# Kernel optimization log

Measured on AMD Instinct MI355X. Metric: run time of the kernel, lower is better.

## Reference

```python
import jax, jax.numpy as jnp
import numpy as np
import math

N, E, G = 10000, 100000, 500
HID, H = 128, 4
C = HID                      # out_channels per head (PyG TransformerConv)
NFREQ, NSPACE = 10, 3
EDIM = 2 * NFREQ * NSPACE    # 60 = dis_emb.dim
LAT, DIS = 6, 3
IN_DIM = HID + LAT + DIS     # 137
EPS = 1e-5


def _lin_init(k, fan_in, shape):
    b = 1.0 / math.sqrt(fan_in)
    return jax.random.uniform(k, shape, jnp.float32, -b, b)


def setup_inputs() -> dict:
    key = jax.random.key(0)
    ks = jax.random.split(key, 12)
    return dict(
        node_features=jax.random.normal(ks[0], (N, HID), jnp.float32),
        frac_coords=jax.random.uniform(ks[1], (N, DIS), jnp.float32),
        lattice_feats=jax.random.normal(ks[2], (G, LAT), jnp.float32),
        edge_index=jax.random.randint(ks[3], (2, E), 0, N),
        node2graph=jnp.sort(jax.random.randint(ks[4], (N,), 0, G)),
        frac_diff=jax.random.normal(ks[5], (E, DIS), jnp.float32) * 0.1,
        ln_gamma=jnp.ones((HID,), jnp.float32),
        ln_beta=jnp.zeros((HID,), jnp.float32),
        Wq=_lin_init(ks[6], IN_DIM, (IN_DIM, H * C)), bq=jnp.zeros((H * C,), jnp.float32),
        Wk=_lin_init(ks[7], IN_DIM, (IN_DIM, H * C)), bk=jnp.zeros((H * C,), jnp.float32),
        Wv=_lin_init(ks[8], IN_DIM, (IN_DIM, H * C)), bv=jnp.zeros((H * C,), jnp.float32),
        We=_lin_init(ks[9], EDIM, (EDIM, H * C)),
        Wskip=_lin_init(ks[10], IN_DIM, (IN_DIM, C)), bskip=jnp.zeros((C,), jnp.float32),
    )


def _sinusoids(frac_diff):
    # SinusoidsEmbedding: emb = x[...,None]*2*pi*arange(F); cat(sin, cos); detached
    freqs = 2.0 * jnp.pi * jnp.arange(NFREQ, dtype=jnp.float32)    # [F]
    emb = frac_diff[:, :, None] * freqs[None, None, :]             # [E,3,F]
    emb = emb.reshape(-1, NSPACE * NFREQ)                          # [E,30]
    return jnp.concatenate([jnp.sin(emb), jnp.cos(emb)], axis=-1)  # [E,60]


def _segment_softmax(scores, idx, num_segments):
    # softmax over variable-size neighborhoods grouped by target node idx
    m = jax.ops.segment_max(scores, idx, num_segments=num_segments)
    ex = jnp.exp(scores - m[idx])
    s = jax.ops.segment_sum(ex, idx, num_segments=num_segments)
    return ex / (s[idx] + 1e-16)


def reference(node_features, frac_coords, lattice_feats, edge_index, node2graph,
              frac_diff, ln_gamma, ln_beta, Wq, bq, Wk, bk, Wv, bv, We, Wskip, bskip):
    edge_emb = jax.lax.stop_gradient(_sinusoids(frac_diff))  # .detach() in original
    node_input = node_features
    # LayerNorm (biased variance, torch default)
    mu = node_features.mean(-1, keepdims=True)
    var = node_features.var(-1, keepdims=True)
    h = (node_features - mu) * jax.lax.rsqrt(var + EPS) * ln_gamma + ln_beta
    # gather per-graph lattice features to nodes, concat
    lat = lattice_feats.reshape(-1, LAT)[node2graph]                # [N,6]
    x = jnp.concatenate([h, lat, frac_coords], axis=1)              # [N,137]

    q = (x @ Wq + bq).reshape(N, H, C)
    k = (x @ Wk + bk).reshape(N, H, C)
    v = (x @ Wv + bv).reshape(N, H, C)
    e = (edge_emb @ We).reshape(E, H, C)                            # lin_edge (no bias)

    src, dst = edge_index[0], edge_index[1]  # message flows src -> dst (PyG default)
    k_e = k[src] + e                                                # [E,H,C]
    alpha = (q[dst] * k_e).sum(-1) / math.sqrt(C)                   # [E,H]
    alpha = _segment_softmax(alpha, dst, N)
    msg = (v[src] + e) * alpha[:, :, None]                          # [E,H,C]
    out = jax.ops.segment_sum(msg, dst, num_segments=N)             # [N,H,C]
    out = out.mean(axis=1)                                          # concat=False -> head mean
    out = out + (x @ Wskip + bskip)                                 # root skip connection
    return node_input + jax.nn.silu(out)
```

## Files before the change

kernel.cpp:

```cpp
#include <hip/hip_runtime.h>
#include <math.h>

#define N_NODES 10000
#define N_EDGES 100000
#define HIDDEN  128
#define NHEAD   4
#define CHAN    128
#define IN_DIM  137
#define KPAD    160
#define NCOLS   1904
#define NPAD    1920
#define LATD    6
#define DISD    3

typedef __attribute__((ext_vector_type(8))) short short8v;
typedef __attribute__((ext_vector_type(4))) float float4v;

__device__ inline unsigned short f2bf(float f) {
    unsigned u = __float_as_uint(f);
    unsigned r = 0x7fffu + ((u >> 16) & 1u);
    return (unsigned short)((u + r) >> 16);
}
__device__ inline float bf2f(unsigned short u) {
    return __uint_as_float(((unsigned)u) << 16);
}

__global__ __launch_bounds__(256) void hist_kernel(
    const int* __restrict__ eidx, int* __restrict__ hist)
{
    int e = blockIdx.x * 256 + threadIdx.x;
    if (e < N_EDGES) atomicAdd(&hist[eidx[N_EDGES + e]], 1);
}

__global__ __launch_bounds__(1024) void scan_kernel(
    const int* __restrict__ hist, int* __restrict__ offsets, int* __restrict__ cursor)
{
    __shared__ int part[1024];
    const int t = threadIdx.x;
    const int base = t * 10;
    int loc[10];
    int s = 0;
    #pragma unroll
    for (int i = 0; i < 10; ++i) {
        int v = (base + i < N_NODES) ? hist[base + i] : 0;
        loc[i] = s; s += v;
    }
    part[t] = s;
    __syncthreads();
    for (int off = 1; off < 1024; off <<= 1) {
        int v = (t >= off) ? part[t - off] : 0;
        __syncthreads();
        part[t] += v;
        __syncthreads();
    }
    int pre = (t > 0) ? part[t - 1] : 0;
    #pragma unroll
    for (int i = 0; i < 10; ++i)
        if (base + i < N_NODES) {
            offsets[base + i] = pre + loc[i];
            cursor[base + i]  = pre + loc[i];
        }
    if (t == 1023) offsets[N_NODES] = part[1023];
}

__global__ __launch_bounds__(256) void scatter_kernel(
    const int* __restrict__ eidx, const float* __restrict__ fdiff,
    int* __restrict__ cursor, int* __restrict__ sorted_src,
    float* __restrict__ sorted_fd)
{
    int e = blockIdx.x * 256 + threadIdx.x;
    if (e >= N_EDGES) return;
    int src = eidx[e];
    int dst = eidx[N_EDGES + e];
    int pos = atomicAdd(&cursor[dst], 1);
    sorted_src[pos] = src;
    sorted_fd[pos * 3 + 0] = fdiff[e * 3 + 0];
    sorted_fd[pos * 3 + 1] = fdiff[e * 3 + 1];
    sorted_fd[pos * 3 + 2] = fdiff[e * 3 + 2];
}

__global__ __launch_bounds__(256) void prep_kernel(
    const float* __restrict__ nf, const float* __restrict__ frac,
    const float* __restrict__ lat, const int* __restrict__ n2g,
    const float* __restrict__ gamma, const float* __restrict__ beta,
    unsigned short* __restrict__ xb, int* __restrict__ hist)
{
    int wave = threadIdx.x >> 6;
    int lane = threadIdx.x & 63;
    int n = blockIdx.x * 4 + wave;
    if (n >= N_NODES) return;

    float v0 = nf[n * HIDDEN + lane];
    float v1 = nf[n * HIDDEN + 64 + lane];
    float s  = v0 + v1;
    float sq = v0 * v0 + v1 * v1;
    #pragma unroll
    for (int m = 1; m < 64; m <<= 1) {
        s  += __shfl_xor(s, m);
        sq += __shfl_xor(sq, m);
    }
    float mean = s * (1.0f / 128.0f);
    float var  = sq * (1.0f / 128.0f) - mean * mean;
    float inv  = rsqrtf(var + 1e-5f);

    xb[n * KPAD + lane]      = f2bf((v0 - mean) * inv * gamma[lane]      + beta[lane]);
    xb[n * KPAD + 64 + lane] = f2bf((v1 - mean) * inv * gamma[64 + lane] + beta[64 + lane]);
    if (lane < LATD) xb[n * KPAD + HIDDEN + lane]        = f2bf(lat[n2g[n] * LATD + lane]);
    if (lane < DISD) xb[n * KPAD + HIDDEN + LATD + lane] = f2bf(frac[n * DISD + lane]);
    if (lane >= 41)  xb[n * KPAD + 96 + lane] = 0;
    if (lane == 0)   hist[n] = 0;
}

__global__ __launch_bounds__(256) void weights_kernel(
    const float* __restrict__ Wq, const float* __restrict__ bq,
    const float* __restrict__ Wk, const float* __restrict__ bk,
    const float* __restrict__ Wv, const float* __restrict__ bv,
    const float* __restrict__ Wsk, const float* __restrict__ bsk,
    const float* __restrict__ We,
    unsigned short* __restrict__ wallT, float* __restrict__ bias_all,
    unsigned short* __restrict__ webt)
{
    int idx = blockIdx.x * 256 + threadIdx.x;
    if (idx < NCOLS * KPAD) {
        int n = idx / KPAD, k = idx % KPAD;
        if (n < 1664) {
            float val = 0.0f;
            if (k < IN_DIM) {
                if (n < 512)        val = Wq[(size_t)k * 512 + n];
                else if (n < 1024)  val = Wk[(size_t)k * 512 + (n - 512)];
                else if (n < 1536)  val = Wv[(size_t)k * 512 + (n - 1024)];
                else                val = Wsk[(size_t)k * 128 + (n - 1536)];
            }
            wallT[idx] = f2bf(val);
            if (k == 0) {
                float b;
                if (n < 512)        b = bq[n];
                else if (n < 1024)  b = bk[n - 512];
                else if (n < 1536)  b = bv[n - 1024];
                else                b = bsk[n - 1536];
                bias_all[n] = b;
            }
        } else {
            int hj = n - 1664;
            int h = hj / 60, j = hj % 60;
            float s = 0.0f;
            if (k < IN_DIM) {
                #pragma unroll 4
                for (int c = 0; c < 128; ++c)
                    s += Wq[(size_t)k * 512 + h * 128 + c] * We[(size_t)j * 512 + h * 128 + c];
            }
            wallT[idx] = f2bf(s);
            if (k == KPAD - 1) {
                float b = 0.0f;
                #pragma unroll 4
                for (int c = 0; c < 128; ++c)
                    b += bq[h * 128 + c] * We[(size_t)j * 512 + h * 128 + c];
                bias_all[n] = b;
            }
        }
    } else {
        int g = idx - NCOLS * KPAD;
        int h = g >> 13, c = (g >> 6) & 127, j = g & 63;
        float v = (j < 60) ? We[(size_t)j * 512 + h * 128 + c] : 0.0f;
        webt[g] = f2bf(v);
    }
}

__global__ __launch_bounds__(256) void mfma_gemm_kernel(
    const unsigned short* __restrict__ xb, const unsigned short* __restrict__ wallT,
    const float* __restrict__ bias_all,
    float* __restrict__ qsq, unsigned short* __restrict__ kvq)
{
    __shared__ __align__(16) unsigned short Alds[64 * 168];
    const int row0 = blockIdx.y * 64;
    const int col0 = blockIdx.x * 128;
    const int tid  = threadIdx.x;

    for (int i = tid; i < 64 * 20; i += 256) {
        int r = i / 20, c8 = (i % 20) * 8;
        uint4 v = make_uint4(0u, 0u, 0u, 0u);
        if (row0 + r < N_NODES)
            v = *reinterpret_cast<const uint4*>(&xb[(size_t)(row0 + r) * KPAD + c8]);
        *reinterpret_cast<uint4*>(&Alds[r * 168 + c8]) = v;
    }
    __syncthreads();

    const int l   = tid & 63;
    const int wid = tid >> 6;
    const int wr  = (wid >> 1) * 32;
    const int wc  = (wid & 1) * 64;
    const int lr  = l & 15;
    const int lk  = (l >> 4) * 8;

    float4v acc[2][4];
    #pragma unroll
    for (int tr = 0; tr < 2; ++tr)
        #pragma unroll
        for (int tc = 0; tc < 4; ++tc)
            acc[tr][tc] = (float4v){0.0f, 0.0f, 0.0f, 0.0f};

    #pragma unroll
    for (int ks = 0; ks < 5; ++ks) {
        short8v a[2], b[4];
        #pragma unroll
        for (int t = 0; t < 2; ++t)
            a[t] = *reinterpret_cast<const short8v*>(&Alds[(wr + t * 16 + lr) * 168 + ks * 32 + lk]);
        #pragma unroll
        for (int t = 0; t < 4; ++t)
            b[t] = *reinterpret_cast<const short8v*>(
                &wallT[(size_t)(col0 + wc + t * 16 + lr) * KPAD + ks * 32 + lk]);
        #pragma unroll
        for (int tr = 0; tr < 2; ++tr)
            #pragma unroll
            for (int tc = 0; tc < 4; ++tc)
                acc[tr][tc] = __builtin_amdgcn_mfma_f32_16x16x32_bf16(a[tr], b[tc], acc[tr][tc], 0, 0, 0);
    }

    #pragma unroll
    for (int tr = 0; tr < 2; ++tr) {
        #pragma unroll
        for (int tc = 0; tc < 4; ++tc) {
            const int col  = col0 + wc + tc * 16 + lr;
            const float bias = bias_all[col];
            #pragma unroll
            for (int j = 0; j < 4; ++j) {
                const int row = row0 + wr + tr * 16 + (l >> 4) * 4 + j;
                if (row < N_NODES) {
                    float val = acc[tr][tc][j] + bias;
                    if (col < 1536)
                        kvq[(size_t)row * 1536 + col] = f2bf(val);
                    else if (col < NCOLS)
                        qsq[(size_t)row * 880 + (col - 1024)] = val;
                }
            }
        }
    }
}

__global__ __launch_bounds__(256) void gather_kernel(
    float* __restrict__ qsq, const unsigned short* __restrict__ kvq,
    const int* __restrict__ offsets, const int* __restrict__ sorted_src,
    const float* __restrict__ sorted_fd)
{
    const int n    = blockIdx.x;
    const int h    = threadIdx.x >> 6;
    const int l    = threadIdx.x & 63;
    const int hl   = l & 31;
    const int half = l >> 5;
    const float TWO_PI = 6.283185307179586f;
    const float scale  = 0.08838834764831845f;

    float* row = qsq + (size_t)n * 880;
    const ushort4 qv = *reinterpret_cast<const ushort4*>(
        &kvq[(size_t)n * 1536 + h * 128 + 4 * hl]);
    const float q4x = bf2f(qv.x), q4y = bf2f(qv.y);
    const float q4z = bf2f(qv.z), q4w = bf2f(qv.w);
    const float qe_a = row[640 + h * 60 + hl];
    const bool  v2ok = (hl < 28);
    const float qe_b = v2ok ? row[640 + h * 60 + hl + 32] : 0.0f;

    const int   jj1  = (hl < 30) ? hl : hl - 30;
    const int   sd1  = jj1 / 10;
    const float fc1  = TWO_PI * (float)(jj1 % 10);
    const bool  sin1 = (hl < 30);
    const int   jj2  = hl + 2;
    const int   sd2  = v2ok ? (jj2 / 10) : 0;
    const float fc2  = v2ok ? TWO_PI * (float)(jj2 % 10) : 0.0f;

    float ax = 0.f, ay = 0.f, az = 0.f, aw = 0.f;
    float agg1 = 0.f, agg2 = 0.f, sumw = 0.f;
    const int e0 = offsets[n], e1 = offsets[n + 1];

    for (int base = e0; base < e1; base += 4) {
        const int eA = base + half;
        const int eB = base + half + 2;
        const bool okA = (eA < e1), okB = (eB < e1);
        const int iA = okA ? eA : e0;
        const int iB = okB ? eB : e0;
        const int srcA = sorted_src[iA];
        const int srcB = sorted_src[iB];
        const float fdA1 = sorted_fd[iA * 3 + sd1];
        const float fdA2 = sorted_fd[iA * 3 + sd2];
        const float fdB1 = sorted_fd[iB * 3 + sd1];
        const float fdB2 = sorted_fd[iB * 3 + sd2];
        const unsigned short* pA = &kvq[(size_t)srcA * 1536 + 512 + h * 128 + 4 * hl];
        const unsigned short* pB = &kvq[(size_t)srcB * 1536 + 512 + h * 128 + 4 * hl];
        const ushort4 kA = *reinterpret_cast<const ushort4*>(pA);
        const ushort4 vA = *reinterpret_cast<const ushort4*>(pA + 512);
        const ushort4 kB = *reinterpret_cast<const ushort4*>(pB);
        const ushort4 vB = *reinterpret_cast<const ushort4*>(pB + 512);

        const float eA1 = sin1 ? __sinf(fdA1 * fc1) : __cosf(fdA1 * fc1);
        const float eA2 = __cosf(fdA2 * fc2);
        const float eB1 = sin1 ? __sinf(fdB1 * fc1) : __cosf(fdB1 * fc1);
        const float eB2 = __cosf(fdB2 * fc2);

        float pAs = q4x * bf2f(kA.x) + q4y * bf2f(kA.y)
                  + q4z * bf2f(kA.z) + q4w * bf2f(kA.w)
                  + eA1 * qe_a + eA2 * qe_b;
        float pBs = q4x * bf2f(kB.x) + q4y * bf2f(kB.y)
                  + q4z * bf2f(kB.z) + q4w * bf2f(kB.w)
                  + eB1 * qe_a + eB2 * qe_b;
        #pragma unroll
        for (int m = 1; m <= 16; m <<= 1) {
            pAs += __shfl_xor(pAs, m);
            pBs += __shfl_xor(pBs, m);
        }
        const float wA = okA ? __expf(pAs * scale) : 0.0f;
        const float wB = okB ? __expf(pBs * scale) : 0.0f;
        sumw += wA + wB;
        ax += wA * bf2f(vA.x) + wB * bf2f(vB.x);
        ay += wA * bf2f(vA.y) + wB * bf2f(vB.y);
        az += wA * bf2f(vA.z) + wB * bf2f(vB.z);
        aw += wA * bf2f(vA.w) + wB * bf2f(vB.w);
        agg1 += wA * eA1 + wB * eB1;
        if (v2ok) agg2 += wA * eA2 + wB * eB2;
    }

    sumw += __shfl_xor(sumw, 32);
    ax += __shfl_xor(ax, 32);  ay += __shfl_xor(ay, 32);
    az += __shfl_xor(az, 32);  aw += __shfl_xor(aw, 32);
    agg1 += __shfl_xor(agg1, 32);
    agg2 += __shfl_xor(agg2, 32);

    __syncthreads();

    if (half == 0) {
        float4 r;
        r.x = ax; r.y = ay; r.z = az; r.w = aw;
        *reinterpret_cast<float4*>(&row[h * 128 + 4 * hl]) = r;
        unsigned short* us = (unsigned short*)(row + 640);
        us[h * 64 + hl]      = f2bf(agg1);
        us[h * 64 + 32 + hl] = f2bf(agg2);
        if (hl == 0) row[768 + h] = sumw;
    }
}

__global__ __launch_bounds__(256) void corr_kernel(
    const unsigned short* __restrict__ webt, float* __restrict__ qsq)
{
    __shared__ __align__(16) unsigned short Alds[32 * 264];
    const int node0 = blockIdx.x * 32;
    const int tid = threadIdx.x;

    for (int i = tid; i < 32 * 32; i += 256) {
        int r = i >> 5, c8 = (i & 31) * 8;
        uint4 v = make_uint4(0u, 0u, 0u, 0u);
        if (node0 + r < N_NODES)
            v = *reinterpret_cast<const uint4*>(
                (const unsigned short*)(qsq + (size_t)(node0 + r) * 880 + 640) + c8);
        *reinterpret_cast<uint4*>(&Alds[r * 264 + c8]) = v;
    }
    __syncthreads();

    const int l  = tid & 63;
    const int h  = tid >> 6;
    const int lr = l & 15;
    const int lk = (l >> 4) * 8;

    float4v acc[2][8];
    #pragma unroll
    for (int m = 0; m < 2; ++m)
        #pragma unroll
        for (int nn = 0; nn < 8; ++nn)
            acc[m][nn] = (float4v){0.0f, 0.0f, 0.0f, 0.0f};

    #pragma unroll
    for (int ks = 0; ks < 2; ++ks) {
        short8v a[2], b[8];
        #pragma unroll
        for (int m = 0; m < 2; ++m)
            a[m] = *reinterpret_cast<const short8v*>(
                &Alds[(m * 16 + lr) * 264 + h * 64 + ks * 32 + lk]);
        #pragma unroll
        for (int nn = 0; nn < 8; ++nn)
            b[nn] = *reinterpret_cast<const short8v*>(
                &webt[(size_t)(h * 128 + nn * 16 + lr) * 64 + ks * 32 + lk]);
        #pragma unroll
        for (int m = 0; m < 2; ++m)
            #pragma unroll
            for (int nn = 0; nn < 8; ++nn)
                acc[m][nn] = __builtin_amdgcn_mfma_f32_16x16x32_bf16(a[m], b[nn], acc[m][nn], 0, 0, 0);
    }

    #pragma unroll
    for (int m = 0; m < 2; ++m) {
        #pragma unroll
        for (int nn = 0; nn < 8; ++nn) {
            const int col = h * 128 + nn * 16 + lr;
            #pragma unroll
            for (int j = 0; j < 4; ++j) {
                const int rowi = node0 + m * 16 + (l >> 4) * 4 + j;
                if (rowi < N_NODES) {
                    float* p = &qsq[(size_t)rowi * 880 + col];
                    *p += acc[m][nn][j];
                }
            }
        }
    }
}

__global__ __launch_bounds__(256) void finalize_kernel(
    const float* __restrict__ qsq, const float* __restrict__ nf,
    float* __restrict__ out)
{
    int idx = blockIdx.x * 256 + threadIdx.x;
    if (idx >= N_NODES * CHAN) return;
    int n = idx >> 7, c = idx & 127;
    const float* row = qsq + (size_t)n * 880;
    float z = 0.0f;
    #pragma unroll
    for (int h = 0; h < NHEAD; ++h)
        z += row[h * 128 + c] / (row[768 + h] + 1e-16f);
    z = 0.25f * z + row[512 + c];
    float si = z / (1.0f + __expf(-z));
    out[idx] = nf[idx] + si;
}

extern "C" void kernel_launch(void* const* d_in, const int* in_sizes, int n_in,
                              void* d_out, int out_size, void* d_ws, size_t ws_size,
                              hipStream_t stream)
{
    const float* nf    = (const float*)d_in[0];
    const float* frac  = (const float*)d_in[1];
    const float* lat   = (const float*)d_in[2];
    const int*   eidx  = (const int*)  d_in[3];
    const int*   n2g   = (const int*)  d_in[4];
    const float* fdiff = (const float*)d_in[5];
    const float* gamma = (const float*)d_in[6];
    const float* beta  = (const float*)d_in[7];
    const float* Wq    = (const float*)d_in[8];
    const float* bq    = (const float*)d_in[9];
    const float* Wk    = (const float*)d_in[10];
    const float* bk    = (const float*)d_in[11];
    const float* Wv    = (const float*)d_in[12];
    const float* bv    = (const float*)d_in[13];
    const float* We    = (const float*)d_in[14];
    const float* Wsk   = (const float*)d_in[15];
    const float* bsk   = (const float*)d_in[16];
    float* out = (float*)d_out;

    float* qsq       = (float*)d_ws;
    float* bias_all  = qsq + (size_t)N_NODES * 880;
    float* sorted_fd = bias_all + NPAD;
    unsigned short* xb    = (unsigned short*)(sorted_fd + (size_t)N_EDGES * 3);
    unsigned short* wallT = xb + (size_t)N_NODES * KPAD;
    unsigned short* webt  = wallT + (size_t)NPAD * KPAD;
    unsigned short* kvq   = webt + 4 * 128 * 64;
    int* hist       = (int*)(kvq + (size_t)N_NODES * 1536);
    int* offsets    = hist + N_NODES;
    int* cursor     = offsets + N_NODES + 1;
    int* sorted_src = cursor + N_NODES;

    prep_kernel<<<(N_NODES + 3) / 4, 256, 0, stream>>>(
        nf, frac, lat, n2g, gamma, beta, xb, hist);
    hist_kernel<<<(N_EDGES + 255) / 256, 256, 0, stream>>>(eidx, hist);
    scan_kernel<<<1, 1024, 0, stream>>>(hist, offsets, cursor);
    scatter_kernel<<<(N_EDGES + 255) / 256, 256, 0, stream>>>(
        eidx, fdiff, cursor, sorted_src, sorted_fd);

    weights_kernel<<<(NCOLS * KPAD + 4 * 128 * 64) / 256, 256, 0, stream>>>(
        Wq, bq, Wk, bk, Wv, bv, Wsk, bsk, We, wallT, bias_all, webt);

    dim3 ggrid(NPAD / 128, (N_NODES + 63) / 64);
    mfma_gemm_kernel<<<ggrid, 256, 0, stream>>>(xb, wallT, bias_all, qsq, kvq);

    gather_kernel<<<N_NODES, 256, 0, stream>>>(
        qsq, kvq, offsets, sorted_src, sorted_fd);

    corr_kernel<<<(N_NODES + 31) / 32, 256, 0, stream>>>(webt, qsq);

    finalize_kernel<<<(N_NODES * CHAN + 255) / 256, 256, 0, stream>>>(
        qsq, nf, out);
}
```

Baseline: 147.7 us.

## Fuse prep with weights packing and corr with finalize, split workspace buffers

Merges the layernorm prep and weight packing into one launch using block-index ranges, and fuses the edge-correction MFMA with the final head-mean, skip-add and SiLU via a shared-memory accumulator. The packed qsq row is split into separate buffers (skip/qe, av, agg, sumw), so gather no longer rewrites the row it reads and its block barrier is removed. This cuts two kernel launches and a full read-modify-write pass over the per-node rows. In exchange, corrfin serialises its four head waves through a phased loop with a barrier per phase.

```diff
diff --git a/kernel.cpp b/kernel.cpp
--- a/kernel.cpp
+++ b/kernel.cpp
@@ -13,6 +13,10 @@
 #define LATD    6
 #define DISD    3
 
+#define PREP_BLOCKS 2500
+#define WTOT   (NCOLS * KPAD + 4 * 128 * 64)
+#define WBLOCKS ((WTOT + 255) / 256)
+
 typedef __attribute__((ext_vector_type(8))) short short8v;
 typedef __attribute__((ext_vector_type(4))) float float4v;
 
@@ -23,6 +27,93 @@
 }
 __device__ inline float bf2f(unsigned short u) {
     return __uint_as_float(((unsigned)u) << 16);
+}
+
+__global__ __launch_bounds__(256) void prep_weights_kernel(
+    const float* __restrict__ nf, const float* __restrict__ frac,
+    const float* __restrict__ lat, const int* __restrict__ n2g,
+    const float* __restrict__ gamma, const float* __restrict__ beta,
+    const float* __restrict__ Wq, const float* __restrict__ bq,
+    const float* __restrict__ Wk, const float* __restrict__ bk,
+    const float* __restrict__ Wv, const float* __restrict__ bv,
+    const float* __restrict__ Wsk, const float* __restrict__ bsk,
+    const float* __restrict__ We,
+    unsigned short* __restrict__ xb, int* __restrict__ hist,
+    unsigned short* __restrict__ wallT, float* __restrict__ bias_all,
+    unsigned short* __restrict__ webt)
+{
+    if (blockIdx.x < PREP_BLOCKS) {
+        int wave = threadIdx.x >> 6;
+        int lane = threadIdx.x & 63;
+        int n = blockIdx.x * 4 + wave;
+        if (n >= N_NODES) return;
+
+        float v0 = nf[n * HIDDEN + lane];
+        float v1 = nf[n * HIDDEN + 64 + lane];
+        float s  = v0 + v1;
+        float sq = v0 * v0 + v1 * v1;
+        #pragma unroll
+        for (int m = 1; m < 64; m <<= 1) {
+            s  += __shfl_xor(s, m);
+            sq += __shfl_xor(sq, m);
+        }
+        float mean = s * (1.0f / 128.0f);
+        float var  = sq * (1.0f / 128.0f) - mean * mean;
+        float inv  = rsqrtf(var + 1e-5f);
+
+        xb[n * KPAD + lane]      = f2bf((v0 - mean) * inv * gamma[lane]      + beta[lane]);
+        xb[n * KPAD + 64 + lane] = f2bf((v1 - mean) * inv * gamma[64 + lane] + beta[64 + lane]);
+        if (lane < LATD) xb[n * KPAD + HIDDEN + lane]        = f2bf(lat[n2g[n] * LATD + lane]);
+        if (lane < DISD) xb[n * KPAD + HIDDEN + LATD + lane] = f2bf(frac[n * DISD + lane]);
+        if (lane >= 41)  xb[n * KPAD + 96 + lane] = 0;
+        if (lane == 0)   hist[n] = 0;
+    } else {
+        int idx = (blockIdx.x - PREP_BLOCKS) * 256 + threadIdx.x;
+        if (idx >= WTOT) return;
+        if (idx < NCOLS * KPAD) {
+            int n = idx / KPAD, k = idx % KPAD;
+            if (n < 1664) {
+                float val = 0.0f;
+                if (k < IN_DIM) {
+                    if (n < 512)        val = Wq[(size_t)k * 512 + n];
+                    else if (n < 1024)  val = Wk[(size_t)k * 512 + (n - 512)];
+                    else if (n < 1536)  val = Wv[(size_t)k * 512 + (n - 1024)];
+                    else                val = Wsk[(size_t)k * 128 + (n - 1536)];
+                }
+                wallT[idx] = f2bf(val);
+                if (k == 0) {
+                    float b;
+                    if (n < 512)        b = bq[n];
+                    else if (n < 1024)  b = bk[n - 512];
+                    else if (n < 1536)  b = bv[n - 1024];
+                    else                b = bsk[n - 1536];
+                    bias_all[n] = b;
+                }
+            } else {
+                int hj = n - 1664;
+                int h = hj / 60, j = hj % 60;
+                float s = 0.0f;
+                if (k < IN_DIM) {
+                    #pragma unroll 4
+                    for (int c = 0; c < 128; ++c)
+                        s += Wq[(size_t)k * 512 + h * 128 + c] * We[(size_t)j * 512 + h * 128 + c];
+                }
+                wallT[idx] = f2bf(s);
+                if (k == KPAD - 1) {
+                    float b = 0.0f;
+                    #pragma unroll 4
+                    for (int c = 0; c < 128; ++c)
+                        b += bq[h * 128 + c] * We[(size_t)j * 512 + h * 128 + c];
+                    bias_all[n] = b;
+                }
+            }
+        } else {
+            int g = idx - NCOLS * KPAD;
+            int h = g >> 13, c = (g >> 6) & 127, j = g & 63;
+            float v = (j < 60) ? We[(size_t)j * 512 + h * 128 + c] : 0.0f;
+            webt[g] = f2bf(v);
+        }
+    }
 }
 
 __global__ __launch_bounds__(256) void hist_kernel(
@@ -79,97 +170,10 @@
     sorted_fd[pos * 3 + 2] = fdiff[e * 3 + 2];
 }
 
-__global__ __launch_bounds__(256) void prep_kernel(
-    const float* __restrict__ nf, const float* __restrict__ frac,
-    const float* __restrict__ lat, const int* __restrict__ n2g,
-    const float* __restrict__ gamma, const float* __restrict__ beta,
-    unsigned short* __restrict__ xb, int* __restrict__ hist)
-{
-    int wave = threadIdx.x >> 6;
-    int lane = threadIdx.x & 63;
-    int n = blockIdx.x * 4 + wave;
-    if (n >= N_NODES) return;
-
-    float v0 = nf[n * HIDDEN + lane];
-    float v1 = nf[n * HIDDEN + 64 + lane];
-    float s  = v0 + v1;
-    float sq = v0 * v0 + v1 * v1;
-    #pragma unroll
-    for (int m = 1; m < 64; m <<= 1) {
-        s  += __shfl_xor(s, m);
-        sq += __shfl_xor(sq, m);
-    }
-    float mean = s * (1.0f / 128.0f);
-    float var  = sq * (1.0f / 128.0f) - mean * mean;
-    float inv  = rsqrtf(var + 1e-5f);
-
-    xb[n * KPAD + lane]      = f2bf((v0 - mean) * inv * gamma[lane]      + beta[lane]);
-    xb[n * KPAD + 64 + lane] = f2bf((v1 - mean) * inv * gamma[64 + lane] + beta[64 + lane]);
-    if (lane < LATD) xb[n * KPAD + HIDDEN + lane]        = f2bf(lat[n2g[n] * LATD + lane]);
-    if (lane < DISD) xb[n * KPAD + HIDDEN + LATD + lane] = f2bf(frac[n * DISD + lane]);
-    if (lane >= 41)  xb[n * KPAD + 96 + lane] = 0;
-    if (lane == 0)   hist[n] = 0;
-}
-
-__global__ __launch_bounds__(256) void weights_kernel(
-    const float* __restrict__ Wq, const float* __restrict__ bq,
-    const float* __restrict__ Wk, const float* __restrict__ bk,
-    const float* __restrict__ Wv, const float* __restrict__ bv,
-    const float* __restrict__ Wsk, const float* __restrict__ bsk,
-    const float* __restrict__ We,
-    unsigned short* __restrict__ wallT, float* __restrict__ bias_all,
-    unsigned short* __restrict__ webt)
-{
-    int idx = blockIdx.x * 256 + threadIdx.x;
-    if (idx < NCOLS * KPAD) {
-        int n = idx / KPAD, k = idx % KPAD;
-        if (n < 1664) {
-            float val = 0.0f;
-            if (k < IN_DIM) {
-                if (n < 512)        val = Wq[(size_t)k * 512 + n];
-                else if (n < 1024)  val = Wk[(size_t)k * 512 + (n - 512)];
-                else if (n < 1536)  val = Wv[(size_t)k * 512 + (n - 1024)];
-                else                val = Wsk[(size_t)k * 128 + (n - 1536)];
-            }
-            wallT[idx] = f2bf(val);
-            if (k == 0) {
-                float b;
-                if (n < 512)        b = bq[n];
-                else if (n < 1024)  b = bk[n - 512];
-                else if (n < 1536)  b = bv[n - 1024];
-                else                b = bsk[n - 1536];
-                bias_all[n] = b;
-            }
-        } else {
-            int hj = n - 1664;
-            int h = hj / 60, j = hj % 60;
-            float s = 0.0f;
-            if (k < IN_DIM) {
-                #pragma unroll 4
-                for (int c = 0; c < 128; ++c)
-                    s += Wq[(size_t)k * 512 + h * 128 + c] * We[(size_t)j * 512 + h * 128 + c];
-            }
-            wallT[idx] = f2bf(s);
-            if (k == KPAD - 1) {
-                float b = 0.0f;
-                #pragma unroll 4
-                for (int c = 0; c < 128; ++c)
-                    b += bq[h * 128 + c] * We[(size_t)j * 512 + h * 128 + c];
-                bias_all[n] = b;
-            }
-        }
-    } else {
-        int g = idx - NCOLS * KPAD;
-        int h = g >> 13, c = (g >> 6) & 127, j = g & 63;
-        float v = (j < 60) ? We[(size_t)j * 512 + h * 128 + c] : 0.0f;
-        webt[g] = f2bf(v);
-    }
-}
-
 __global__ __launch_bounds__(256) void mfma_gemm_kernel(
     const unsigned short* __restrict__ xb, const unsigned short* __restrict__ wallT,
     const float* __restrict__ bias_all,
-    float* __restrict__ qsq, unsigned short* __restrict__ kvq)
+    float* __restrict__ sq, unsigned short* __restrict__ kvq)
 {
     __shared__ __align__(16) unsigned short Alds[64 * 168];
     const int row0 = blockIdx.y * 64;
@@ -229,8 +233,10 @@
                     float val = acc[tr][tc][j] + bias;
                     if (col < 1536)
                         kvq[(size_t)row * 1536 + col] = f2bf(val);
+                    else if (col < 1664)
+                        sq[(size_t)row * 384 + (col - 1536)] = val;
                     else if (col < NCOLS)
-                        qsq[(size_t)row * 880 + (col - 1024)] = val;
+                        sq[(size_t)row * 384 + 128 + (col - 1664)] = val;
                 }
             }
         }
@@ -238,9 +244,11 @@
 }
 
 __global__ __launch_bounds__(256) void gather_kernel(
-    float* __restrict__ qsq, const unsigned short* __restrict__ kvq,
+    const float* __restrict__ sq, const unsigned short* __restrict__ kvq,
     const int* __restrict__ offsets, const int* __restrict__ sorted_src,
-    const float* __restrict__ sorted_fd)
+    const float* __restrict__ sorted_fd,
+    float* __restrict__ avbuf, unsigned short* __restrict__ aggbuf,
+    float* __restrict__ sumwbuf)
 {
     const int n    = blockIdx.x;
     const int h    = threadIdx.x >> 6;
@@ -250,14 +258,13 @@
     const float TWO_PI = 6.283185307179586f;
     const float scale  = 0.08838834764831845f;
 
-    float* row = qsq + (size_t)n * 880;
     const ushort4 qv = *reinterpret_cast<const ushort4*>(
         &kvq[(size_t)n * 1536 + h * 128 + 4 * hl]);
     const float q4x = bf2f(qv.x), q4y = bf2f(qv.y);
     const float q4z = bf2f(qv.z), q4w = bf2f(qv.w);
-    const float qe_a = row[640 + h * 60 + hl];
+    const float qe_a = sq[(size_t)n * 384 + 128 + h * 60 + hl];
     const bool  v2ok = (hl < 28);
-    const float qe_b = v2ok ? row[640 + h * 60 + hl + 32] : 0.0f;
+    const float qe_b = v2ok ? sq[(size_t)n * 384 + 128 + h * 60 + hl + 32] : 0.0f;
 
     const int   jj1  = (hl < 30) ? hl : hl - 30;
     const int   sd1  = jj1 / 10;
@@ -323,23 +330,24 @@
     agg1 += __shfl_xor(agg1, 32);
     agg2 += __shfl_xor(agg2, 32);
 
-    __syncthreads();
-
     if (half == 0) {
         float4 r;
         r.x = ax; r.y = ay; r.z = az; r.w = aw;
-        *reinterpret_cast<float4*>(&row[h * 128 + 4 * hl]) = r;
-        unsigned short* us = (unsigned short*)(row + 640);
-        us[h * 64 + hl]      = f2bf(agg1);
-        us[h * 64 + 32 + hl] = f2bf(agg2);
-        if (hl == 0) row[768 + h] = sumw;
-    }
-}
-
-__global__ __launch_bounds__(256) void corr_kernel(
-    const unsigned short* __restrict__ webt, float* __restrict__ qsq)
+        *reinterpret_cast<float4*>(&avbuf[(size_t)n * 512 + h * 128 + 4 * hl]) = r;
+        aggbuf[n * 256 + h * 64 + hl]      = f2bf(agg1);
+        aggbuf[n * 256 + h * 64 + 32 + hl] = f2bf(agg2);
+        if (hl == 0) sumwbuf[n * 4 + h] = sumw;
+    }
+}
+
+__global__ __launch_bounds__(256) void corrfin_kernel(
+    const unsigned short* __restrict__ webt, const unsigned short* __restrict__ aggbuf,
+    const float* __restrict__ avbuf, const float* __restrict__ sumwbuf,
+    const float* __restrict__ sq, const float* __restrict__ nf,
+    float* __restrict__ out)
 {
     __shared__ __align__(16) unsigned short Alds[32 * 264];
+    __shared__ float zbuf[32 * 128];
     const int node0 = blockIdx.x * 32;
     const int tid = threadIdx.x;
 
@@ -347,10 +355,10 @@
         int r = i >> 5, c8 = (i & 31) * 8;
         uint4 v = make_uint4(0u, 0u, 0u, 0u);
         if (node0 + r < N_NODES)
-            v = *reinterpret_cast<const uint4*>(
-                (const unsigned short*)(qsq + (size_t)(node0 + r) * 880 + 640) + c8);
+            v = *reinterpret_cast<const uint4*>(&aggbuf[(size_t)(node0 + r) * 256 + c8]);
         *reinterpret_cast<uint4*>(&Alds[r * 264 + c8]) = v;
     }
+    for (int i = tid; i < 32 * 128; i += 256) zbuf[i] = 0.0f;
     __syncthreads();
 
     const int l  = tid & 63;
@@ -383,38 +391,39 @@
                 acc[m][nn] = __builtin_amdgcn_mfma_f32_16x16x32_bf16(a[m], b[nn], acc[m][nn], 0, 0, 0);
     }
 
-    #pragma unroll
-    for (int m = 0; m < 2; ++m) {
-        #pragma unroll
-        for (int nn = 0; nn < 8; ++nn) {
-            const int col = h * 128 + nn * 16 + lr;
+    for (int ph = 0; ph < 4; ++ph) {
+        if (ph == h) {
             #pragma unroll
-            for (int j = 0; j < 4; ++j) {
-                const int rowi = node0 + m * 16 + (l >> 4) * 4 + j;
-                if (rowi < N_NODES) {
-                    float* p = &qsq[(size_t)rowi * 880 + col];
-                    *p += acc[m][nn][j];
+            for (int m = 0; m < 2; ++m) {
+                #pragma unroll
+                for (int nn = 0; nn < 8; ++nn) {
+                    const int col = nn * 16 + lr;
+                    #pragma unroll
+                    for (int j = 0; j < 4; ++j) {
+                        const int r = m * 16 + (l >> 4) * 4 + j;
+                        const int gn = node0 + r;
+                        if (gn < N_NODES) {
+                            const float sw = sumwbuf[gn * 4 + h] + 1e-16f;
+                            const float val = (avbuf[(size_t)gn * 512 + h * 128 + col]
+                                               + acc[m][nn][j]) / sw;
+                            zbuf[r * 128 + col] += val;
+                        }
+                    }
                 }
             }
         }
-    }
-}
-
-__global__ __launch_bounds__(256) void finalize_kernel(
-    const float* __restrict__ qsq, const float* __restrict__ nf,
-    float* __restrict__ out)
-{
-    int idx = blockIdx.x * 256 + threadIdx.x;
-    if (idx >= N_NODES * CHAN) return;
-    int n = idx >> 7, c = idx & 127;
-    const float* row = qsq + (size_t)n * 880;
-    float z = 0.0f;
-    #pragma unroll
-    for (int h = 0; h < NHEAD; ++h)
-        z += row[h * 128 + c] / (row[768 + h] + 1e-16f);
-    z = 0.25f * z + row[512 + c];
-    float si = z / (1.0f + __expf(-z));
-    out[idx] = nf[idx] + si;
+        __syncthreads();
+    }
+
+    for (int i = tid; i < 32 * 128; i += 256) {
+        const int r = i >> 7, c = i & 127;
+        const int gn = node0 + r;
+        if (gn < N_NODES) {
+            float z = 0.25f * zbuf[i] + sq[(size_t)gn * 384 + c];
+            float si = z / (1.0f + __expf(-z));
+            out[gn * CHAN + c] = nf[gn * CHAN + c] + si;
+        }
+    }
 }
 
 extern "C" void kernel_launch(void* const* d_in, const int* in_sizes, int n_in,
@@ -440,36 +449,37 @@
     const float* bsk   = (const float*)d_in[16];
     float* out = (float*)d_out;
 
-    float* qsq       = (float*)d_ws;
-    float* bias_all  = qsq + (size_t)N_NODES * 880;
+    float* sq        = (float*)d_ws;
+    float* avbuf     = sq + (size_t)N_NODES * 384;
+    float* sumwbuf   = avbuf + (size_t)N_NODES * 512;
+    float* bias_all  = sumwbuf + (size_t)N_NODES * 4;
     float* sorted_fd = bias_all + NPAD;
-    unsigned short* xb    = (unsigned short*)(sorted_fd + (size_t)N_EDGES * 3);
-    unsigned short* wallT = xb + (size_t)N_NODES * KPAD;
-    unsigned short* webt  = wallT + (size_t)NPAD * KPAD;
-    unsigned short* kvq   = webt + 4 * 128 * 64;
+    unsigned short* xb     = (unsigned short*)(sorted_fd + (size_t)N_EDGES * 3);
+    unsigned short* wallT  = xb + (size_t)N_NODES * KPAD;
+    unsigned short* webt   = wallT + (size_t)NPAD * KPAD;
+    unsigned short* aggbuf = webt + 4 * 128 * 64;
+    unsigned short* kvq    = aggbuf + (size_t)N_NODES * 256;
     int* hist       = (int*)(kvq + (size_t)N_NODES * 1536);
     int* offsets    = hist + N_NODES;
     int* cursor     = offsets + N_NODES + 1;
     int* sorted_src = cursor + N_NODES;
 
-    prep_kernel<<<(N_NODES + 3) / 4, 256, 0, stream>>>(
-        nf, frac, lat, n2g, gamma, beta, xb, hist);
+    prep_weights_kernel<<<PREP_BLOCKS + WBLOCKS, 256, 0, stream>>>(
+        nf, frac, lat, n2g, gamma, beta,
+        Wq, bq, Wk, bk, Wv, bv, Wsk, bsk, We,
+        xb, hist, wallT, bias_all, webt);
+
     hist_kernel<<<(N_EDGES + 255) / 256, 256, 0, stream>>>(eidx, hist);
     scan_kernel<<<1, 1024, 0, stream>>>(hist, offsets, cursor);
     scatter_kernel<<<(N_EDGES + 255) / 256, 256, 0, stream>>>(
         eidx, fdiff, cursor, sorted_src, sorted_fd);
 
-    weights_kernel<<<(NCOLS * KPAD + 4 * 128 * 64) / 256, 256, 0, stream>>>(
-        Wq, bq, Wk, bk, Wv, bv, Wsk, bsk, We, wallT, bias_all, webt);
-
     dim3 ggrid(NPAD / 128, (N_NODES + 63) / 64);
-    mfma_gemm_kernel<<<ggrid, 256, 0, stream>>>(xb, wallT, bias_all, qsq, kvq);
+    mfma_gemm_kernel<<<ggrid, 256, 0, stream>>>(xb, wallT, bias_all, sq, kvq);
 
     gather_kernel<<<N_NODES, 256, 0, stream>>>(
-        qsq, kvq, offsets, sorted_src, sorted_fd);
-
-    corr_kernel<<<(N_NODES + 31) / 32, 256, 0, stream>>>(webt, qsq);
-
-    finalize_kernel<<<(N_NODES * CHAN + 255) / 256, 256, 0, stream>>>(
-        qsq, nf, out);
-}
+        sq, kvq, offsets, sorted_src, sorted_fd, avbuf, aggbuf, sumwbuf);
+
+    corrfin_kernel<<<(N_NODES + 31) / 32, 256, 0, stream>>>(
+        webt, aggbuf, avbuf, sumwbuf, sq, nf, out);
+}
```

After: 193.4 us. 1.31x slower.
